# Optimization experiments

Hardware: AMD Instinct MI355X
Metric: run time of the kernel (lower is better)

## Reference

```python
import jax, jax.numpy as jnp
import numpy as np

K = 20
EPS = 1e-5
SLOPE = 0.2


def _leaky(v):
    return jnp.where(v >= 0, v, SLOPE * v)


def _instnorm(v, axes):
    # InstanceNorm with affine=False: normalize per (batch, channel) over spatial axes,
    # biased variance, eps=1e-5 (torch default).
    mean = jnp.mean(v, axis=axes, keepdims=True)
    var = jnp.mean((v - mean) ** 2, axis=axes, keepdims=True)
    return (v - mean) * jax.lax.rsqrt(var + EPS)


def _knn_idx(x, k):
    # x: [B, C, N]; returns indices of k nearest neighbors (self included), [B, N, k]
    inner = -2.0 * jnp.einsum('bcn,bcm->bnm', x, x)
    xx = jnp.sum(x * x, axis=1)                      # [B, N]
    pd = -xx[:, :, None] - inner - xx[:, None, :]    # negative squared distance
    return jax.lax.top_k(pd, k)[1]


def _edge_conv(x, w):
    # x: [B, C, N]; w: [O, 2C]. Returns [B, O, N] after max-pool over k neighbors.
    B, C, N = x.shape
    idx = _knn_idx(x, K)                              # [B, N, K]
    xt = jnp.transpose(x, (0, 2, 1))                  # [B, N, C]
    b_idx = jnp.arange(B)[:, None, None]
    nb = xt[b_idx, idx]                               # [B, N, K, C] gathered neighbors
    ctr = xt[:, :, None, :]                           # [B, N, 1, C]
    feat = jnp.concatenate([nb - ctr, jnp.broadcast_to(ctr, nb.shape)], axis=-1)
    h = jnp.einsum('oc,bnkc->bonk', w, feat)          # 1x1 conv as GEMM -> [B, O, N, K]
    h = _leaky(_instnorm(h, (2, 3)))
    return jnp.max(h, axis=-1)                        # [B, O, N]


def setup_inputs() -> dict:
    key = jax.random.key(0)
    ks = jax.random.split(key, 6)
    B, N, feat_dim = 8, 2048, 512
    return {
        'x': jax.random.normal(ks[0], (B, N, 3), dtype=jnp.float32),
        'w1': jax.random.normal(ks[1], (64, 6), dtype=jnp.float32) * 0.1,
        'w2': jax.random.normal(ks[2], (64, 128), dtype=jnp.float32) * 0.1,
        'w3': jax.random.normal(ks[3], (128, 128), dtype=jnp.float32) * 0.1,
        'w4': jax.random.normal(ks[4], (256, 256), dtype=jnp.float32) * 0.1,
        'w5': jax.random.normal(ks[5], (feat_dim, 512), dtype=jnp.float32) * 0.1,
    }


def reference(x, w1, w2, w3, w4, w5):
    xc = jnp.transpose(x, (0, 2, 1))                  # [B, 3, N]
    x1 = _edge_conv(xc, w1)                           # [B, 64, N]
    x2 = _edge_conv(x1, w2)                           # [B, 64, N]
    x3 = _edge_conv(x2, w3)                           # [B, 128, N]
    x4 = _edge_conv(x3, w4)                           # [B, 256, N]
    cat = jnp.concatenate([x1, x2, x3, x4], axis=1)   # [B, 512, N]
    h = jnp.einsum('oc,bcn->bon', w5, cat)            # conv5 (1x1 conv1d)
    feat = _leaky(_instnorm(h, (2,)))
    return feat                                       # [B, feat_dim, N]
```

## Files before the change

### kernel.cpp

```cpp
#include <hip/hip_runtime.h>
#include <math.h>

#define NPTS 2048
#define NB 8
#define KNN 20
#define EPSI 1e-5f
#define SLOPE 0.2f
#define CHUNK 512

typedef short bf16x8 __attribute__((ext_vector_type(8)));
typedef float f32x4 __attribute__((ext_vector_type(4)));

__device__ __forceinline__ unsigned short f2bf(float x) {
    union { float f; unsigned u; } v; v.f = x;
    unsigned r = v.u + 0x7FFF + ((v.u >> 16) & 1u);
    return (unsigned short)(r >> 16);
}
__device__ __forceinline__ float bf2f(unsigned short h) {
    union { unsigned u; float f; } v; v.u = ((unsigned)h) << 16; return v.f;
}

__device__ __forceinline__ void gl_lds16(const unsigned short* g, unsigned short* l) {
    __builtin_amdgcn_global_load_lds(
        (const __attribute__((address_space(1))) void*)g,
        (__attribute__((address_space(3))) void*)l, 16, 0, 0);
}

__global__ __launch_bounds__(256) void transpose_kernel(const float* __restrict__ xin,
                                                        float* __restrict__ xc) {
    int g = blockIdx.x * 256 + threadIdx.x;
    int b = g / NPTS, n = g % NPTS;
    float v0 = xin[(size_t)g * 3 + 0];
    float v1 = xin[(size_t)g * 3 + 1];
    float v2 = xin[(size_t)g * 3 + 2];
    xc[((size_t)b * 3 + 0) * NPTS + n] = v0;
    xc[((size_t)b * 3 + 1) * NPTS + n] = v1;
    xc[((size_t)b * 3 + 2) * NPTS + n] = v2;
}

__global__ __launch_bounds__(256) void xx_kernel(const float* __restrict__ x, int bstride, int C,
                                                 float* __restrict__ xx) {
    int g = blockIdx.x * 256 + threadIdx.x;
    int b = g / NPTS, n = g % NPTS;
    const float* p = x + (size_t)b * bstride + n;
    float s = 0.f;
    for (int c = 0; c < C; ++c) { float v = p[(size_t)c * NPTS]; s += v * v; }
    xx[g] = s;
}

__global__ __launch_bounds__(256) void pd_gemm3(const float* __restrict__ x, int bstride, int C,
                                                const float* __restrict__ xx,
                                                float* __restrict__ pd, int r0) {
    __shared__ float As[2][16][128];
    __shared__ float Bs[2][16][128];
    int b = blockIdx.z;
    int nbase_l = blockIdx.y * 128;
    int mbase = blockIdx.x * 128;
    int tx = threadIdx.x & 15, ty = threadIdx.x >> 4;
    int tid = threadIdx.x;
    float acc[8][8] = {};
    const float* xb = x + (size_t)b * bstride;

    {
        int KC = min(16, C);
        for (int t = tid; t < 512; t += 256) {
            int cc = t >> 5, j4 = (t & 31) * 4;
            float4 av = make_float4(0.f, 0.f, 0.f, 0.f), bv = av;
            if (cc < KC) {
                av = *(const float4*)&xb[(size_t)cc * NPTS + r0 + nbase_l + j4];
                bv = *(const float4*)&xb[(size_t)cc * NPTS + mbase + j4];
            }
            *(float4*)&As[0][cc][j4] = av;
            *(float4*)&Bs[0][cc][j4] = bv;
        }
    }
    __syncthreads();

    int cur = 0;
    for (int c0 = 0; c0 < C; c0 += 16) {
        int c1 = c0 + 16;
        if (c1 < C) {
            int KC = min(16, C - c1);
            for (int t = tid; t < 512; t += 256) {
                int cc = t >> 5, j4 = (t & 31) * 4;
                float4 av = make_float4(0.f, 0.f, 0.f, 0.f), bv = av;
                if (cc < KC) {
                    av = *(const float4*)&xb[(size_t)(c1 + cc) * NPTS + r0 + nbase_l + j4];
                    bv = *(const float4*)&xb[(size_t)(c1 + cc) * NPTS + mbase + j4];
                }
                *(float4*)&As[cur ^ 1][cc][j4] = av;
                *(float4*)&Bs[cur ^ 1][cc][j4] = bv;
            }
        }
        int KC = min(16, C - c0);
        if (KC == 16) {
            #pragma unroll
            for (int cc = 0; cc < 16; ++cc) {
                float av[8], bv[8];
                *(float4*)&av[0] = *(const float4*)&As[cur][cc][ty * 8];
                *(float4*)&av[4] = *(const float4*)&As[cur][cc][ty * 8 + 4];
                *(float4*)&bv[0] = *(const float4*)&Bs[cur][cc][tx * 4];
                *(float4*)&bv[4] = *(const float4*)&Bs[cur][cc][64 + tx * 4];
                #pragma unroll
                for (int i = 0; i < 8; ++i)
                    #pragma unroll
                    for (int j = 0; j < 8; ++j)
                        acc[i][j] += av[i] * bv[j];
            }
        } else {
            for (int cc = 0; cc < KC; ++cc) {
                float av[8], bv[8];
                *(float4*)&av[0] = *(const float4*)&As[cur][cc][ty * 8];
                *(float4*)&av[4] = *(const float4*)&As[cur][cc][ty * 8 + 4];
                *(float4*)&bv[0] = *(const float4*)&Bs[cur][cc][tx * 4];
                *(float4*)&bv[4] = *(const float4*)&Bs[cur][cc][64 + tx * 4];
                #pragma unroll
                for (int i = 0; i < 8; ++i)
                    #pragma unroll
                    for (int j = 0; j < 8; ++j)
                        acc[i][j] += av[i] * bv[j];
            }
        }
        __syncthreads();
        cur ^= 1;
    }

    const float* xxb = xx + (size_t)b * NPTS;
    #pragma unroll
    for (int i = 0; i < 8; ++i) {
        int nl = nbase_l + ty * 8 + i;
        float xn = xxb[r0 + nl];
        float4 o0, o1;
        o0.x = 2.f * acc[i][0] - xn - xxb[mbase + tx*4 + 0];
        o0.y = 2.f * acc[i][1] - xn - xxb[mbase + tx*4 + 1];
        o0.z = 2.f * acc[i][2] - xn - xxb[mbase + tx*4 + 2];
        o0.w = 2.f * acc[i][3] - xn - xxb[mbase + tx*4 + 3];
        o1.x = 2.f * acc[i][4] - xn - xxb[mbase + 64 + tx*4 + 0];
        o1.y = 2.f * acc[i][5] - xn - xxb[mbase + 64 + tx*4 + 1];
        o1.z = 2.f * acc[i][6] - xn - xxb[mbase + 64 + tx*4 + 2];
        o1.w = 2.f * acc[i][7] - xn - xxb[mbase + 64 + tx*4 + 3];
        *(float4*)&pd[((size_t)b * CHUNK + nl) * NPTS + mbase + tx*4] = o0;
        *(float4*)&pd[((size_t)b * CHUNK + nl) * NPTS + mbase + 64 + tx*4] = o1;
    }
}

__global__ __launch_bounds__(256) void topk_kernel(const float* __restrict__ pd,
                                                   int* __restrict__ idxout, int r0) {
    int wid = (blockIdx.x * 256 + threadIdx.x) >> 6;
    int lane = threadIdx.x & 63;
    int b = wid / CHUNK;
    int nl = wid % CHUNK;
    int n = r0 + nl;
    const float* row = pd + ((size_t)b * CHUNK + nl) * NPTS;

    float v[32];
    #pragma unroll
    for (int j = 0; j < 32; ++j) v[j] = row[lane + 64 * j];

    unsigned mask = 0u;
    int saved = 0;
    for (int t = 0; t < KNN; ++t) {
        float best = -INFINITY; int bj = 0;
        #pragma unroll
        for (int j = 0; j < 32; ++j) {
            bool ok = ((mask >> j) & 1u) == 0u;
            if (ok && v[j] > best) { best = v[j]; bj = j; }
        }
        int midx = lane + 64 * bj;
        #pragma unroll
        for (int off = 32; off > 0; off >>= 1) {
            float ov = __shfl_xor(best, off);
            int om = __shfl_xor(midx, off);
            if (ov > best || (ov == best && om < midx)) { best = ov; midx = om; }
        }
        if (lane == t) saved = midx;
        if ((midx & 63) == lane) mask |= 1u << (midx >> 6);
    }
    if (lane < KNN) idxout[((size_t)b * NPTS + n) * KNN + lane] = saved;
}

__global__ __launch_bounds__(256) void yz_gemm2(const float* __restrict__ x, int bstride, int C, int O,
                                                const float* __restrict__ w,
                                                float* __restrict__ y, float* __restrict__ z) {
    __shared__ float Xs[32][64];
    __shared__ float Wd[32][68];
    __shared__ float Wz[32][68];
    int b = blockIdx.z;
    int mbase = blockIdx.x * 64;
    int obase = blockIdx.y * 64;
    int tid = threadIdx.x;
    int nq = tid & 15, oq = tid >> 4;
    const float* xb = x + (size_t)b * bstride;
    int C2 = 2 * C;
    float accy[4][4] = {}, accz[4][4] = {};

    for (int c0 = 0; c0 < C; c0 += 32) {
        int KC = min(32, C - c0);
        for (int t = tid; t < 512; t += 256) {
            int cc = t >> 4, j4 = (t & 15) * 4;
            float4 v = make_float4(0.f, 0.f, 0.f, 0.f);
            if (cc < KC) v = *(const float4*)&xb[(size_t)(c0 + cc) * NPTS + mbase + j4];
            *(float4*)&Xs[cc][j4] = v;
        }
        for (int t = tid; t < 2048; t += 256) {
            int o = t >> 5, cc = t & 31;
            float wd = 0.f, wz = 0.f;
            if (cc < KC) {
                wd = w[(size_t)(obase + o) * C2 + c0 + cc];
                wz = w[(size_t)(obase + o) * C2 + C + c0 + cc] - wd;
            }
            Wd[cc][o] = wd; Wz[cc][o] = wz;
        }
        __syncthreads();
        for (int cc = 0; cc < KC; ++cc) {
            float xv[4], wdv[4], wzv[4];
            *(float4*)xv  = *(float4*)&Xs[cc][nq * 4];
            *(float4*)wdv = *(float4*)&Wd[cc][oq * 4];
            *(float4*)wzv = *(float4*)&Wz[cc][oq * 4];
            #pragma unroll
            for (int i = 0; i < 4; ++i)
                #pragma unroll
                for (int j = 0; j < 4; ++j) {
                    accy[i][j] += wdv[i] * xv[j];
                    accz[i][j] += wzv[i] * xv[j];
                }
        }
        __syncthreads();
    }

    #pragma unroll
    for (int i = 0; i < 4; ++i) {
        size_t off = ((size_t)b * O + obase + oq * 4 + i) * NPTS + mbase + nq * 4;
        *(float4*)&y[off] = make_float4(accy[i][0], accy[i][1], accy[i][2], accy[i][3]);
        *(float4*)&z[off] = make_float4(accz[i][0], accz[i][1], accz[i][2], accz[i][3]);
    }
}

__global__ __launch_bounds__(256) void gather_norm2(const float* __restrict__ y,
                                                    const float* __restrict__ z,
                                                    const int* __restrict__ idx,
                                                    float* __restrict__ cat, int coff, int O) {
    __shared__ float yt[NPTS][4];
    __shared__ float red[32];
    int og = blockIdx.x * 4, b = blockIdx.y;
    int tid = threadIdx.x;

    for (int n = tid; n < NPTS; n += 256) {
        float4 v;
        v.x = y[((size_t)b * O + og + 0) * NPTS + n];
        v.y = y[((size_t)b * O + og + 1) * NPTS + n];
        v.z = y[((size_t)b * O + og + 2) * NPTS + n];
        v.w = y[((size_t)b * O + og + 3) * NPTS + n];
        *(float4*)&yt[n][0] = v;
    }
    __syncthreads();

    float s1[4] = {0.f, 0.f, 0.f, 0.f}, s2[4] = {0.f, 0.f, 0.f, 0.f};
    float hm[4][8];
    for (int r = 0; r < 8; ++r) {
        int n = r * 256 + tid;
        const int* ip = idx + ((size_t)b * NPTS + n) * KNN;
        float zv[4], mx[4];
        #pragma unroll
        for (int j = 0; j < 4; ++j) {
            zv[j] = z[((size_t)b * O + og + j) * NPTS + n];
            mx[j] = -INFINITY;
        }
        #pragma unroll
        for (int k = 0; k < KNN; ++k) {
            int id = ip[k];
            float4 yv = *(float4*)&yt[id][0];
            float h0 = yv.x + zv[0]; s1[0] += h0; s2[0] += h0 * h0; mx[0] = fmaxf(mx[0], h0);
            float h1 = yv.y + zv[1]; s1[1] += h1; s2[1] += h1 * h1; mx[1] = fmaxf(mx[1], h1);
            float h2 = yv.z + zv[2]; s1[2] += h2; s2[2] += h2 * h2; mx[2] = fmaxf(mx[2], h2);
            float h3 = yv.w + zv[3]; s1[3] += h3; s2[3] += h3 * h3; mx[3] = fmaxf(mx[3], h3);
        }
        #pragma unroll
        for (int j = 0; j < 4; ++j) hm[j][r] = mx[j];
    }
    #pragma unroll
    for (int off = 32; off > 0; off >>= 1)
        #pragma unroll
        for (int j = 0; j < 4; ++j) {
            s1[j] += __shfl_xor(s1[j], off);
            s2[j] += __shfl_xor(s2[j], off);
        }
    int wv = tid >> 6, lane = tid & 63;
    if (lane == 0)
        #pragma unroll
        for (int j = 0; j < 4; ++j) { red[j * 8 + wv] = s1[j]; red[j * 8 + 4 + wv] = s2[j]; }
    __syncthreads();
    const float inv = 1.f / (float)(NPTS * KNN);
    #pragma unroll
    for (int j = 0; j < 4; ++j) {
        float S1 = red[j * 8 + 0] + red[j * 8 + 1] + red[j * 8 + 2] + red[j * 8 + 3];
        float S2 = red[j * 8 + 4] + red[j * 8 + 5] + red[j * 8 + 6] + red[j * 8 + 7];
        float mean = S1 * inv;
        float var = S2 * inv - mean * mean;
        float rs = 1.f / sqrtf(var + EPSI);
        float* dst = cat + ((size_t)b * 512 + coff + og + j) * NPTS;
        #pragma unroll
        for (int r = 0; r < 8; ++r) {
            float vv = (hm[j][r] - mean) * rs;
            dst[r * 256 + tid] = vv >= 0.f ? vv : SLOPE * vv;
        }
    }
}

__global__ __launch_bounds__(256) void w5_prep(const float* __restrict__ w5,
                                               unsigned short* __restrict__ wcat) {
    int i = blockIdx.x * 256 + threadIdx.x;
    int o = i >> 9, c = i & 511;
    float x = w5[i];
    unsigned short h = f2bf(x);
    wcat[(size_t)o * 1024 + c] = h;
    wcat[(size_t)o * 1024 + 512 + c] = f2bf(x - bf2f(h));
}

__global__ __launch_bounds__(256) void catT_prep(const float* __restrict__ cat,
                                                 unsigned short* __restrict__ ct) {
    __shared__ float t[32][33];
    int b = blockIdx.z;
    int n0 = blockIdx.x * 32, c0 = blockIdx.y * 32;
    int tx = threadIdx.x & 31, ty = threadIdx.x >> 5;
    #pragma unroll
    for (int r = 0; r < 4; ++r) {
        int ci = ty + r * 8;
        t[ci][tx] = cat[((size_t)b * 512 + c0 + ci) * NPTS + n0 + tx];
    }
    __syncthreads();
    #pragma unroll
    for (int r = 0; r < 4; ++r) {
        int ni = ty + r * 8;
        float x = t[tx][ni];
        unsigned short h = f2bf(x);
        size_t off = ((size_t)b * NPTS + n0 + ni) * 1024 + c0 + tx;
        ct[off] = h;
        ct[off + 512] = f2bf(x - bf2f(h));
    }
}

__global__ __launch_bounds__(256, 2) void final_gemm_mfma2(const unsigned short* __restrict__ wcat,
                                                           const unsigned short* __restrict__ ct,
                                                           float* __restrict__ h) {
    __shared__ unsigned short smem[4 * 8192];
    int b = blockIdx.z;
    int nbase = blockIdx.x * 128, obase = blockIdx.y * 128;
    int tid = threadIdx.x;
    int w = tid >> 6, l = tid & 63;
    int wr = (w >> 1) * 64, wc = (w & 1) * 64;
    int lr = l & 15, lq = l >> 4;

    const unsigned short* Ag = wcat + (size_t)obase * 1024;
    const unsigned short* Bg = ct + ((size_t)b * NPTS + nbase) * 1024;

    int rw = l >> 3, g = l & 7, sg = g ^ rw;

    f32x4 acc[4][4] = {};

    auto STAGE = [&](int buf, int k0) {
        unsigned short* Ad = smem + buf * 16384;
        unsigned short* Bd = Ad + 8192;
        #pragma unroll
        for (int pass = 0; pass < 4; ++pass) {
            int rbase = pass * 32 + w * 8;
            int row = rbase + rw;
            gl_lds16(Ag + (size_t)row * 1024 + k0 + sg * 8, Ad + rbase * 64);
            gl_lds16(Bg + (size_t)row * 1024 + k0 + sg * 8, Bd + rbase * 64);
        }
    };

    STAGE(0, 0);
    __syncthreads();

    int cur = 0;
    for (int kt = 0; kt < 16; ++kt) {
        if (kt < 15) STAGE(cur ^ 1, (kt + 1) * 64);
        const unsigned short* As = smem + cur * 16384;
        const unsigned short* Bs = As + 8192;
        #pragma unroll
        for (int kk = 0; kk < 2; ++kk) {
            bf16x8 af[4], bf[4];
            int gl = kk * 4 + lq;
            #pragma unroll
            for (int mi = 0; mi < 4; ++mi) {
                int row = wr + mi * 16 + lr;
                af[mi] = *(const bf16x8*)&As[row * 64 + ((gl ^ (row & 7)) * 8)];
            }
            #pragma unroll
            for (int ni = 0; ni < 4; ++ni) {
                int row = wc + ni * 16 + lr;
                bf[ni] = *(const bf16x8*)&Bs[row * 64 + ((gl ^ (row & 7)) * 8)];
            }
            #pragma unroll
            for (int mi = 0; mi < 4; ++mi)
                #pragma unroll
                for (int ni = 0; ni < 4; ++ni)
                    acc[mi][ni] = __builtin_amdgcn_mfma_f32_16x16x32_bf16(af[mi], bf[ni], acc[mi][ni], 0, 0, 0);
        }
        __syncthreads();
        cur ^= 1;
    }

    int orow0 = obase + wr + lq * 4;
    int ncol0 = nbase + wc + lr;
    #pragma unroll
    for (int mi = 0; mi < 4; ++mi)
        #pragma unroll
        for (int r = 0; r < 4; ++r)
            #pragma unroll
            for (int ni = 0; ni < 4; ++ni)
                h[((size_t)b * 512 + orow0 + mi * 16 + r) * NPTS + ncol0 + ni * 16] = acc[mi][ni][r];
}

__global__ __launch_bounds__(256) void final_norm(const float* __restrict__ h,
                                                  float* __restrict__ out) {
    __shared__ float red[8];
    int o = blockIdx.x, b = blockIdx.y;
    int tid = threadIdx.x;
    const float* hr = h + ((size_t)b * 512 + o) * NPTS;
    float s1 = 0.f, s2 = 0.f;
    float v[8];
    #pragma unroll
    for (int r = 0; r < 8; ++r) {
        v[r] = hr[r * 256 + tid];
        s1 += v[r]; s2 += v[r] * v[r];
    }
    #pragma unroll
    for (int off = 32; off > 0; off >>= 1) {
        s1 += __shfl_xor(s1, off);
        s2 += __shfl_xor(s2, off);
    }
    int wv = tid >> 6, lane = tid & 63;
    if (lane == 0) { red[wv] = s1; red[4 + wv] = s2; }
    __syncthreads();
    float S1 = red[0] + red[1] + red[2] + red[3];
    float S2 = red[4] + red[5] + red[6] + red[7];
    const float inv = 1.f / (float)NPTS;
    float mean = S1 * inv;
    float var = S2 * inv - mean * mean;
    float rs = 1.f / sqrtf(var + EPSI);
    float* dst = out + ((size_t)b * 512 + o) * NPTS;
    #pragma unroll
    for (int r = 0; r < 8; ++r) {
        float vv = (v[r] - mean) * rs;
        dst[r * 256 + tid] = vv >= 0.f ? vv : SLOPE * vv;
    }
}

extern "C" void kernel_launch(void* const* d_in, const int* in_sizes, int n_in,
                              void* d_out, int out_size, void* d_ws, size_t ws_size,
                              hipStream_t stream) {
    const float* x_in = (const float*)d_in[0];
    const float* w1 = (const float*)d_in[1];
    const float* w2 = (const float*)d_in[2];
    const float* w3 = (const float*)d_in[3];
    const float* w4 = (const float*)d_in[4];
    const float* w5 = (const float*)d_in[5];
    float* out = (float*)d_out;
    float* ws = (float*)d_ws;

    float* region = ws;
    float* yb = region;
    float* zb = region + 4194304;
    float* pdb = region;
    int* idxb = (int*)(ws + 8388608);
    float* xxb = ws + 8388608 + 327680;
    float* xcb = xxb + NB * NPTS;
    float* cat = xcb + NB * 3 * NPTS;
    unsigned short* wcat = (unsigned short*)(cat + 8388608);
    unsigned short* ct = (unsigned short*)region;
    float* hb = cat;

    transpose_kernel<<<NB * NPTS / 256, 256, 0, stream>>>(x_in, xcb);
    w5_prep<<<512 * 512 / 256, 256, 0, stream>>>(w5, wcat);

    const float* srcs[4] = {xcb, cat, cat + (size_t)64 * NPTS, cat + (size_t)128 * NPTS};
    int bstr[4] = {3 * NPTS, 512 * NPTS, 512 * NPTS, 512 * NPTS};
    int Cin[4] = {3, 64, 64, 128};
    int Oc[4] = {64, 64, 128, 256};
    const float* wl[4] = {w1, w2, w3, w4};
    int coffs[4] = {0, 64, 128, 256};

    for (int li = 0; li < 4; ++li) {
        xx_kernel<<<NB * NPTS / 256, 256, 0, stream>>>(srcs[li], bstr[li], Cin[li], xxb);
        for (int r0 = 0; r0 < NPTS; r0 += CHUNK) {
            pd_gemm3<<<dim3(NPTS / 128, CHUNK / 128, NB), 256, 0, stream>>>(
                srcs[li], bstr[li], Cin[li], xxb, pdb, r0);
            topk_kernel<<<NB * CHUNK / 4, 256, 0, stream>>>(pdb, idxb, r0);
        }
        yz_gemm2<<<dim3(NPTS / 64, Oc[li] / 64, NB), 256, 0, stream>>>(
            srcs[li], bstr[li], Cin[li], Oc[li], wl[li], yb, zb);
        gather_norm2<<<dim3(Oc[li] / 4, NB), 256, 0, stream>>>(yb, zb, idxb, cat, coffs[li], Oc[li]);
    }

    catT_prep<<<dim3(NPTS / 32, 512 / 32, NB), 256, 0, stream>>>(cat, ct);
    final_gemm_mfma2<<<dim3(NPTS / 128, 512 / 128, NB), 256, 0, stream>>>(wcat, ct, hb);
    final_norm<<<dim3(512, NB), 256, 0, stream>>>(hb, out);
}
```

Baseline: 1.327 ms.

## Fuse pairwise-distance GEMM with top-k into a single kNN kernel

Replaces the chunked pd_gemm3 + topk_kernel pair with one kernel that computes 16 query rows' distances to all points tile by tile, staging each tile in LDS and keeping each row's 2048 distances in registers before running the warp top-k. This removes the large pairwise-distance matrix write/read through global memory and the repeated launches per chunk. In exchange the GEMM reuse is much lower (16 rows per block, 4 outputs per thread), so every block re-streams the full feature matrix, and register pressure rises from holding two 32-element rows per lane. For C=3, the 32-channel tile load reads past the 3 valid channels, touching memory beyond the input rows, though the extra values are not used in the sum.

```diff
diff --git a/kernel.cpp b/kernel.cpp
--- a/kernel.cpp
+++ b/kernel.cpp
@@ -6,7 +6,6 @@
 #define KNN 20
 #define EPSI 1e-5f
 #define SLOPE 0.2f
-#define CHUNK 512
 
 typedef short bf16x8 __attribute__((ext_vector_type(8)));
 typedef float f32x4 __attribute__((ext_vector_type(4)));
@@ -21,6 +20,11 @@
 }
 
 __device__ __forceinline__ void gl_lds16(const unsigned short* g, unsigned short* l) {
+    __builtin_amdgcn_global_load_lds(
+        (const __attribute__((address_space(1))) void*)g,
+        (__attribute__((address_space(3))) void*)l, 16, 0, 0);
+}
+__device__ __forceinline__ void gl_lds16f(const float* g, float* l) {
     __builtin_amdgcn_global_load_lds(
         (const __attribute__((address_space(1))) void*)g,
         (__attribute__((address_space(3))) void*)l, 16, 0, 0);
@@ -48,135 +52,101 @@
     xx[g] = s;
 }
 
-__global__ __launch_bounds__(256) void pd_gemm3(const float* __restrict__ x, int bstride, int C,
-                                                const float* __restrict__ xx,
-                                                float* __restrict__ pd, int r0) {
-    __shared__ float As[2][16][128];
-    __shared__ float Bs[2][16][128];
-    int b = blockIdx.z;
-    int nbase_l = blockIdx.y * 128;
-    int mbase = blockIdx.x * 128;
-    int tx = threadIdx.x & 15, ty = threadIdx.x >> 4;
+__global__ __launch_bounds__(512, 4) void knn_fused2(const float* __restrict__ x, int bstride, int C,
+                                                     const float* __restrict__ xx,
+                                                     int* __restrict__ idxout) {
+    __shared__ float As[128][16];
+    __shared__ float Bs[2][32][128];
+    __shared__ float pdt[16][132];
+    int b = blockIdx.y;
+    int R0 = blockIdx.x * 16;
     int tid = threadIdx.x;
-    float acc[8][8] = {};
+    int row = tid & 15, colq = tid >> 4;
+    int w = tid >> 6, l = tid & 63;
     const float* xb = x + (size_t)b * bstride;
-
-    {
-        int KC = min(16, C);
-        for (int t = tid; t < 512; t += 256) {
-            int cc = t >> 5, j4 = (t & 31) * 4;
-            float4 av = make_float4(0.f, 0.f, 0.f, 0.f), bv = av;
-            if (cc < KC) {
-                av = *(const float4*)&xb[(size_t)cc * NPTS + r0 + nbase_l + j4];
-                bv = *(const float4*)&xb[(size_t)cc * NPTS + mbase + j4];
-            }
-            *(float4*)&As[0][cc][j4] = av;
-            *(float4*)&Bs[0][cc][j4] = bv;
-        }
-    }
-    __syncthreads();
-
-    int cur = 0;
-    for (int c0 = 0; c0 < C; c0 += 16) {
-        int c1 = c0 + 16;
-        if (c1 < C) {
-            int KC = min(16, C - c1);
-            for (int t = tid; t < 512; t += 256) {
-                int cc = t >> 5, j4 = (t & 31) * 4;
-                float4 av = make_float4(0.f, 0.f, 0.f, 0.f), bv = av;
-                if (cc < KC) {
-                    av = *(const float4*)&xb[(size_t)(c1 + cc) * NPTS + r0 + nbase_l + j4];
-                    bv = *(const float4*)&xb[(size_t)(c1 + cc) * NPTS + mbase + j4];
+    const float* xxb = xx + (size_t)b * NPTS;
+
+    for (int f = tid; f < C * 4; f += 512) {
+        int c = f >> 2, i = (f & 3) * 4;
+        *(float4*)&As[c][i] = *(const float4*)&xb[(size_t)c * NPTS + R0 + i];
+    }
+
+    float v[2][32];
+    int KCH = (C + 31) >> 5;
+    float xr = xxb[R0 + row];
+
+    #pragma unroll
+    for (int ct = 0; ct < 16; ++ct) {
+        int M0 = ct * 128;
+        #pragma unroll
+        for (int s = 0; s < 2; ++s) {
+            int f = s * 2048 + tid * 4;
+            int c = f >> 7, col = f & 127;
+            gl_lds16f(xb + (size_t)c * NPTS + M0 + col, &Bs[0][0][0] + f);
+        }
+        float acc0 = 0.f, acc1 = 0.f, acc2 = 0.f, acc3 = 0.f;
+        __syncthreads();
+        int cur = 0;
+        for (int kidx = 0; kidx < KCH; ++kidx) {
+            if (kidx + 1 < KCH) {
+                int c0n = (kidx + 1) * 32;
+                #pragma unroll
+                for (int s = 0; s < 2; ++s) {
+                    int f = s * 2048 + tid * 4;
+                    int c = f >> 7, col = f & 127;
+                    gl_lds16f(xb + (size_t)(c0n + c) * NPTS + M0 + col, &Bs[cur ^ 1][0][0] + f);
                 }
-                *(float4*)&As[cur ^ 1][cc][j4] = av;
-                *(float4*)&Bs[cur ^ 1][cc][j4] = bv;
-            }
-        }
-        int KC = min(16, C - c0);
-        if (KC == 16) {
-            #pragma unroll
-            for (int cc = 0; cc < 16; ++cc) {
-                float av[8], bv[8];
-                *(float4*)&av[0] = *(const float4*)&As[cur][cc][ty * 8];
-                *(float4*)&av[4] = *(const float4*)&As[cur][cc][ty * 8 + 4];
-                *(float4*)&bv[0] = *(const float4*)&Bs[cur][cc][tx * 4];
-                *(float4*)&bv[4] = *(const float4*)&Bs[cur][cc][64 + tx * 4];
-                #pragma unroll
-                for (int i = 0; i < 8; ++i)
-                    #pragma unroll
-                    for (int j = 0; j < 8; ++j)
-                        acc[i][j] += av[i] * bv[j];
-            }
-        } else {
+            }
+            int c0 = kidx * 32;
+            int KC = min(32, C - c0);
             for (int cc = 0; cc < KC; ++cc) {
-                float av[8], bv[8];
-                *(float4*)&av[0] = *(const float4*)&As[cur][cc][ty * 8];
-                *(float4*)&av[4] = *(const float4*)&As[cur][cc][ty * 8 + 4];
-                *(float4*)&bv[0] = *(const float4*)&Bs[cur][cc][tx * 4];
-                *(float4*)&bv[4] = *(const float4*)&Bs[cur][cc][64 + tx * 4];
-                #pragma unroll
-                for (int i = 0; i < 8; ++i)
-                    #pragma unroll
-                    for (int j = 0; j < 8; ++j)
-                        acc[i][j] += av[i] * bv[j];
-            }
-        }
-        __syncthreads();
-        cur ^= 1;
-    }
-
-    const float* xxb = xx + (size_t)b * NPTS;
-    #pragma unroll
-    for (int i = 0; i < 8; ++i) {
-        int nl = nbase_l + ty * 8 + i;
-        float xn = xxb[r0 + nl];
-        float4 o0, o1;
-        o0.x = 2.f * acc[i][0] - xn - xxb[mbase + tx*4 + 0];
-        o0.y = 2.f * acc[i][1] - xn - xxb[mbase + tx*4 + 1];
-        o0.z = 2.f * acc[i][2] - xn - xxb[mbase + tx*4 + 2];
-        o0.w = 2.f * acc[i][3] - xn - xxb[mbase + tx*4 + 3];
-        o1.x = 2.f * acc[i][4] - xn - xxb[mbase + 64 + tx*4 + 0];
-        o1.y = 2.f * acc[i][5] - xn - xxb[mbase + 64 + tx*4 + 1];
-        o1.z = 2.f * acc[i][6] - xn - xxb[mbase + 64 + tx*4 + 2];
-        o1.w = 2.f * acc[i][7] - xn - xxb[mbase + 64 + tx*4 + 3];
-        *(float4*)&pd[((size_t)b * CHUNK + nl) * NPTS + mbase + tx*4] = o0;
-        *(float4*)&pd[((size_t)b * CHUNK + nl) * NPTS + mbase + 64 + tx*4] = o1;
-    }
-}
-
-__global__ __launch_bounds__(256) void topk_kernel(const float* __restrict__ pd,
-                                                   int* __restrict__ idxout, int r0) {
-    int wid = (blockIdx.x * 256 + threadIdx.x) >> 6;
-    int lane = threadIdx.x & 63;
-    int b = wid / CHUNK;
-    int nl = wid % CHUNK;
-    int n = r0 + nl;
-    const float* row = pd + ((size_t)b * CHUNK + nl) * NPTS;
-
-    float v[32];
-    #pragma unroll
-    for (int j = 0; j < 32; ++j) v[j] = row[lane + 64 * j];
-
-    unsigned mask = 0u;
-    int saved = 0;
-    for (int t = 0; t < KNN; ++t) {
-        float best = -INFINITY; int bj = 0;
-        #pragma unroll
-        for (int j = 0; j < 32; ++j) {
-            bool ok = ((mask >> j) & 1u) == 0u;
-            if (ok && v[j] > best) { best = v[j]; bj = j; }
-        }
-        int midx = lane + 64 * bj;
-        #pragma unroll
-        for (int off = 32; off > 0; off >>= 1) {
-            float ov = __shfl_xor(best, off);
-            int om = __shfl_xor(midx, off);
-            if (ov > best || (ov == best && om < midx)) { best = ov; midx = om; }
-        }
-        if (lane == t) saved = midx;
-        if ((midx & 63) == lane) mask |= 1u << (midx >> 6);
-    }
-    if (lane < KNN) idxout[((size_t)b * NPTS + n) * KNN + lane] = saved;
+                float a = As[c0 + cc][row];
+                float4 bv = *(const float4*)&Bs[cur][cc][colq * 4];
+                acc0 += a * bv.x; acc1 += a * bv.y; acc2 += a * bv.z; acc3 += a * bv.w;
+            }
+            __syncthreads();
+            cur ^= 1;
+        }
+        {
+            int cb = M0 + colq * 4;
+            float4 o;
+            o.x = 2.f * acc0 - xr - xxb[cb + 0];
+            o.y = 2.f * acc1 - xr - xxb[cb + 1];
+            o.z = 2.f * acc2 - xr - xxb[cb + 2];
+            o.w = 2.f * acc3 - xr - xxb[cb + 3];
+            *(float4*)&pdt[row][colq * 4] = o;
+        }
+        __syncthreads();
+        v[0][2 * ct]     = pdt[2 * w][l];
+        v[0][2 * ct + 1] = pdt[2 * w][64 + l];
+        v[1][2 * ct]     = pdt[2 * w + 1][l];
+        v[1][2 * ct + 1] = pdt[2 * w + 1][64 + l];
+        __syncthreads();
+    }
+
+    #pragma unroll
+    for (int k = 0; k < 2; ++k) {
+        unsigned mask = 0u;
+        int saved = 0;
+        for (int t = 0; t < KNN; ++t) {
+            float best = -INFINITY; int bj = 0;
+            #pragma unroll
+            for (int j = 0; j < 32; ++j) {
+                bool ok = ((mask >> j) & 1u) == 0u;
+                if (ok && v[k][j] > best) { best = v[k][j]; bj = j; }
+            }
+            int midx = l + 64 * bj;
+            #pragma unroll
+            for (int off = 32; off > 0; off >>= 1) {
+                float ov = __shfl_xor(best, off);
+                int om = __shfl_xor(midx, off);
+                if (ov > best || (ov == best && om < midx)) { best = ov; midx = om; }
+            }
+            if (l == t) saved = midx;
+            if ((midx & 63) == l) mask |= 1u << (midx >> 6);
+        }
+        if (l < KNN) idxout[((size_t)b * NPTS + R0 + 2 * w + k) * KNN + l] = saved;
+    }
 }
 
 __global__ __launch_bounds__(256) void yz_gemm2(const float* __restrict__ x, int bstride, int C, int O,
@@ -463,7 +433,6 @@
     float* region = ws;
     float* yb = region;
     float* zb = region + 4194304;
-    float* pdb = region;
     int* idxb = (int*)(ws + 8388608);
     float* xxb = ws + 8388608 + 327680;
     float* xcb = xxb + NB * NPTS;
@@ -484,11 +453,7 @@
 
     for (int li = 0; li < 4; ++li) {
         xx_kernel<<<NB * NPTS / 256, 256, 0, stream>>>(srcs[li], bstr[li], Cin[li], xxb);
-        for (int r0 = 0; r0 < NPTS; r0 += CHUNK) {
-            pd_gemm3<<<dim3(NPTS / 128, CHUNK / 128, NB), 256, 0, stream>>>(
-                srcs[li], bstr[li], Cin[li], xxb, pdb, r0);
-            topk_kernel<<<NB * CHUNK / 4, 256, 0, stream>>>(pdb, idxb, r0);
-        }
+        knn_fused2<<<dim3(NPTS / 16, NB), 512, 0, stream>>>(srcs[li], bstr[li], Cin[li], xxb, idxb);
         yz_gemm2<<<dim3(NPTS / 64, Oc[li] / 64, NB), 256, 0, stream>>>(
             srcs[li], bstr[li], Cin[li], Oc[li], wl[li], yb, zb);
         gather_norm2<<<dim3(Oc[li] / 4, NB), 256, 0, stream>>>(yb, zb, idxb, cat, coffs[li], Oc[li]);
```

Result: slower. 1.358 ms (+2.3%).
